# Kernel tuning notes

Measured on AMD Instinct MI355X. Metric: run time of the kernel, lower is better.

## Reference

```python
import jax, jax.numpy as jnp
import numpy as np

N_NODES = 20000
N_EDGES = 320000
IN_DIM = 256
OUT_DIM = 256
N_HEADS = 4
D_K = OUT_DIM // N_HEADS
N_NTYPES = 4
N_RELS = 8
SQRT_DK = float(np.sqrt(D_K))


def setup_inputs() -> dict:
    key = jax.random.key(0)
    ks = jax.random.split(key, 12)
    xav = lambda k, shape, fan: jax.random.normal(k, shape, jnp.float32) * (1.0 / np.sqrt(fan))
    return {
        "h": jax.random.normal(ks[0], (N_NODES, IN_DIM), jnp.float32),
        "k_linears": xav(ks[1], (N_NTYPES, IN_DIM, OUT_DIM), IN_DIM),
        "q_linears": xav(ks[2], (N_NTYPES, IN_DIM, OUT_DIM), IN_DIM),
        "v_linears": xav(ks[3], (N_NTYPES, IN_DIM, OUT_DIM), IN_DIM),
        "a_linears": xav(ks[4], (N_NTYPES, OUT_DIM, OUT_DIM), OUT_DIM),
        "relation_att": xav(ks[5], (N_RELS, N_HEADS, D_K, D_K), D_K),
        "relation_msg": xav(ks[6], (N_RELS, N_HEADS, D_K, D_K), D_K),
        "relation_pri": jnp.ones((N_RELS, N_HEADS), jnp.float32),
        "skip": jnp.ones((N_NTYPES,), jnp.float32),
        "node_type": jax.random.randint(ks[7], (N_NODES,), 0, N_NTYPES),
        "etype": jnp.sort(jax.random.randint(ks[8], (N_EDGES,), 0, N_RELS)),
        "row_idx": jax.random.randint(ks[9], (N_EDGES,), 0, N_NODES),
        "col_idx": jax.random.randint(ks[10], (N_EDGES,), 0, N_NODES),
    }


def _typed_matmul(x, W, node_type):
    # x: [N, in], W: [T, in, out] -> per-node-type projection [N, out]
    all_t = jnp.einsum("ni,tio->tno", x, W)  # [T, N, out]
    return all_t[node_type, jnp.arange(x.shape[0])]


def reference(h, k_linears, q_linears, v_linears, a_linears,
              relation_att, relation_msg, relation_pri, skip,
              node_type, etype, row_idx, col_idx):
    n = h.shape[0]
    # per-node-type K/Q/V projections -> [N, H, d_k]
    k = _typed_matmul(h, k_linears, node_type).reshape(n, N_HEADS, D_K)
    q = _typed_matmul(h, q_linears, node_type).reshape(n, N_HEADS, D_K)
    v = _typed_matmul(h, v_linears, node_type).reshape(n, N_HEADS, D_K)

    # per-relation transforms computed at node granularity, gathered per edge
    q_att = jnp.einsum("nhd,rhde->rnhe", q, relation_att)  # [R, N, H, d_k]
    v_msg = jnp.einsum("nhd,rhde->rnhe", v, relation_msg)  # [R, N, H, d_k]

    aw_q_edge = q_att[etype, col_idx]   # [E, H, d_k]  (dst-side q transformed by rel att)
    msg_edge = v_msg[etype, row_idx]    # [E, H, d_k]  (src-side v transformed by rel msg)

    # attention score: <rel_att @ q_dst, k_src> * pri_r / sqrt(d_k)  -> [E, H]
    attn_score = jnp.sum(aw_q_edge * k[row_idx], axis=-1)
    score = attn_score * (relation_pri[etype] / SQRT_DK)

    # edge softmax over incoming edges of each destination node
    m = jax.ops.segment_max(score, col_idx, num_segments=n)       # [N, H]
    ex = jnp.exp(score - m[col_idx])                              # [E, H]
    denom = jax.ops.segment_sum(ex, col_idx, num_segments=n)      # [N, H]
    alpha = ex / denom[col_idx]                                   # [E, H]

    agg = jax.ops.segment_sum(alpha[..., None] * msg_edge, col_idx,
                              num_segments=n)                     # [N, H, d_k]
    agg = agg.reshape(n, OUT_DIM)

    # output per-node-type projection scaled by sigmoid(skip[type])
    out = _typed_matmul(agg, a_linears, node_type)
    out = jax.nn.sigmoid(skip)[node_type][:, None] * out
    return out
```

## Files before the change

kernel.cpp:

```cpp
#include <hip/hip_runtime.h>

static constexpr int NN  = 20000;
static constexpr int NE  = 320000;
static constexpr int NTY = 4;
static constexpr int NRL = 8;
static constexpr int NB  = NRL * NN;

static constexpr int ZB   = (NB + NN * 4 + 255) / 256;
static constexpr int CB   = (NN + 255) / 256;
static constexpr int WSEG = 192;
static constexpr int ASEG = 64;
static constexpr int RSEG = 32;

typedef short bf16x8 __attribute__((ext_vector_type(8)));
typedef float f32x4  __attribute__((ext_vector_type(4)));
typedef unsigned short u16x4 __attribute__((ext_vector_type(4)));

__device__ __forceinline__ unsigned short f2bf(float f) {
  unsigned u = __float_as_uint(f);
  u += 0x7fffu + ((u >> 16) & 1u);
  return (unsigned short)(u >> 16);
}
__device__ __forceinline__ float bf2f(unsigned short b) {
  return __uint_as_float(((unsigned)b) << 16);
}
__device__ __forceinline__ f32x4 mfma16(bf16x8 a, bf16x8 b, f32x4 c) {
  return __builtin_amdgcn_mfma_f32_16x16x32_bf16(a, b, c, 0, 0, 0);
}

__global__ void k_prep_all(const float* __restrict__ Wk, const float* __restrict__ Wq,
                           const float* __restrict__ Wv, const float* __restrict__ Wa,
                           const float* __restrict__ ratt, const float* __restrict__ rmsg,
                           const int* __restrict__ ntype,
                           int* bcnt, float* denom, int* c4p,
                           unsigned short* Wt, unsigned short* At,
                           unsigned short* Att, unsigned short* Mt) {
  __shared__ float tl[64][65];
  __shared__ int cc[4];
  int b = blockIdx.x, tid = threadIdx.x;
  if (b < ZB) {
    int i = b * 256 + tid;
    if (i < NB) bcnt[i] = 0;
    else if (i < NB + NN * 4) denom[i - NB] = 0.f;
    return;
  }
  b -= ZB;
  if (b < CB) {
    if (tid < 4) cc[tid] = 0;
    __syncthreads();
    int i = b * 256 + tid;
    if (i < NN) atomicAdd(&cc[ntype[i]], 1);
    __syncthreads();
    if (tid < 4) c4p[b * 4 + tid] = cc[tid];
    return;
  }
  b -= CB;
  int r4 = tid >> 6, c = tid & 63;
  if (b < WSEG) {
    int mat = b >> 4, tile = b & 15;
    int t = mat / 3, w = mat % 3;
    const float* src = (w == 0) ? Wk : (w == 1) ? Wq : Wv;
    src += (size_t)t * 65536;
    int ti = (tile >> 2) * 64, tj = (tile & 3) * 64;
#pragma unroll
    for (int p = 0; p < 16; ++p) {
      int row = p * 4 + r4;
      tl[row][c] = src[(size_t)(ti + row) * 256 + tj + c];
    }
    __syncthreads();
#pragma unroll
    for (int p = 0; p < 16; ++p) {
      int jr = p * 4 + r4;
      Wt[((size_t)(t * 768 + w * 256 + tj + jr)) * 256 + ti + c] = f2bf(tl[c][jr]);
    }
    return;
  }
  b -= WSEG;
  if (b < ASEG) {
    int t = b >> 4, tile = b & 15;
    int ti = (tile >> 2) * 64, tj = (tile & 3) * 64;
#pragma unroll
    for (int p = 0; p < 16; ++p) {
      int row = p * 4 + r4;
      tl[row][c] = Wa[(size_t)(t * 256 + ti + row) * 256 + tj + c];
    }
    __syncthreads();
#pragma unroll
    for (int p = 0; p < 16; ++p) {
      int jr = p * 4 + r4;
      At[((size_t)(t * 256 + tj + jr)) * 256 + ti + c] = f2bf(tl[c][jr]);
    }
    return;
  }
  b -= ASEG;
  {
    int rh = b;
#pragma unroll
    for (int p = 0; p < 16; ++p) {
      int d = p * 4 + r4;
      tl[d][c] = ratt[(size_t)rh * 4096 + d * 64 + c];
    }
    __syncthreads();
#pragma unroll
    for (int p = 0; p < 16; ++p) {
      int e = p * 4 + r4;
      Att[(size_t)rh * 4096 + e * 64 + c] = f2bf(tl[c][e]);
    }
    __syncthreads();
#pragma unroll
    for (int p = 0; p < 16; ++p) {
      int d = p * 4 + r4;
      tl[d][c] = rmsg[(size_t)rh * 4096 + d * 64 + c];
    }
    __syncthreads();
#pragma unroll
    for (int p = 0; p < 16; ++p) {
      int e = p * 4 + r4;
      Mt[(size_t)rh * 4096 + e * 64 + c] = f2bf(tl[c][e]);
    }
  }
}

__global__ void k_meta(const int* __restrict__ c4p, int* toff, int* ncur,
                       int* mt64_t, int* mt64_m, int* gcnt) {
  __shared__ int c4[4];
  __shared__ int ts[5];
  if (threadIdx.x < 4) {
    int s = 0;
    for (int b = 0; b < CB; ++b) s += c4p[b * 4 + threadIdx.x];
    c4[threadIdx.x] = s;
  }
  __syncthreads();
  if (threadIdx.x == 0) {
    int s = 0, s2 = 0;
    for (int t = 0; t < NTY; ++t) {
      toff[t] = s; ncur[t] = s; s += c4[t];
      ts[t] = s2; s2 += (c4[t] + 63) >> 6;
    }
    toff[NTY] = s; ts[NTY] = s2; gcnt[0] = s2;
  }
  __syncthreads();
  int n64 = ts[4];
  for (int i = threadIdx.x; i < n64; i += 256) {
    int t = 0;
    while (t < 3 && i >= ts[t + 1]) ++t;
    mt64_t[i] = t; mt64_m[i] = i - ts[t];
  }
}
__global__ void k_nscatter(const int* __restrict__ key, int* cur,
                           int* nperm, int* inv) {
  int i = blockIdx.x * 256 + threadIdx.x;
  if (i < NN) {
    int p = atomicAdd(&cur[key[i]], 1);
    nperm[p] = i;
    inv[i] = p;
  }
}

__global__ void k_bcount(const int* __restrict__ etyp, const int* __restrict__ coli,
                         const int* __restrict__ inv, int* bcnt) {
  int e = blockIdx.x * 256 + threadIdx.x;
  if (e < NE) atomicAdd(&bcnt[etyp[e] * NN + inv[coli[e]]], 1);
}
__global__ void k_scan1(const int* cnt, int* off, int* psum) {
  __shared__ int sm[256];
  int i = blockIdx.x * 256 + threadIdx.x;
  int v = cnt[i];
  sm[threadIdx.x] = v;
  __syncthreads();
  for (int d = 1; d < 256; d <<= 1) {
    int t = (threadIdx.x >= d) ? sm[threadIdx.x - d] : 0;
    __syncthreads();
    sm[threadIdx.x] += t;
    __syncthreads();
  }
  off[i] = sm[threadIdx.x] - v;
  if (threadIdx.x == 255) psum[blockIdx.x] = sm[255];
}
__global__ void k_scan2(int* psum) {
  __shared__ int sm[1024];
  int t = threadIdx.x;
  int v = (t < 625) ? psum[t] : 0;
  sm[t] = v;
  __syncthreads();
  for (int d = 1; d < 1024; d <<= 1) {
    int x = (t >= d) ? sm[t - d] : 0;
    __syncthreads();
    sm[t] += x;
    __syncthreads();
  }
  if (t < 625) psum[t] = sm[t] - v;
}
__global__ void k_scan3(int* off, int* cur, const int* psum) {
  int i = blockIdx.x * 256 + threadIdx.x;
  int v = off[i] + psum[blockIdx.x];
  off[i] = v; cur[i] = v;
  if (i == 0) off[NB] = NE;
}
__global__ void k_escatter(const int* __restrict__ etyp, const int* __restrict__ rowi,
                           const int* __restrict__ coli, const int* __restrict__ inv,
                           int* cur, int* je) {
  int e = blockIdx.x * 256 + threadIdx.x;
  if (e >= NE) return;
  int bin = etyp[e] * NN + inv[coli[e]];
  int j = atomicAdd(&cur[bin], 1);
  je[j] = inv[rowi[e]];
}

__global__ __launch_bounds__(256) void k_gemm_kqv(
    const float* __restrict__ hsrc, const unsigned short* __restrict__ Wt,
    const int* __restrict__ nperm, const int* __restrict__ toff,
    const int* __restrict__ mt64_t, const int* __restrict__ mt64_m,
    const int* __restrict__ gcnt,
    unsigned short* __restrict__ kvb, unsigned short* __restrict__ qb) {
  __shared__ unsigned short bs[16][264];
  int mtile = blockIdx.x / 3, chunk = blockIdx.x % 3;
  if (mtile >= gcnt[0]) return;
  int wave = threadIdx.x >> 6, lane = threadIdx.x & 63;
  int t = mt64_t[mtile], tm = mt64_m[mtile];
  int base = toff[t], cnt = toff[t + 1] - base;
  int lr = lane & 15, kq = lane >> 4;
  int arow = tm * 64 + wave * 16 + lr;
  int prow = base + (arow < cnt ? arow : cnt - 1);
  int node = nperm[prow];
  const float* ap = hsrc + (size_t)node * 256 + kq * 8;
  bf16x8 af[8];
#pragma unroll
  for (int s = 0; s < 8; ++s) {
    f32x4 x0 = *(const f32x4*)(ap + s * 32);
    f32x4 x1 = *(const f32x4*)(ap + s * 32 + 4);
    bf16x8 o;
    o[0] = (short)f2bf(x0[0]); o[1] = (short)f2bf(x0[1]);
    o[2] = (short)f2bf(x0[2]); o[3] = (short)f2bf(x0[3]);
    o[4] = (short)f2bf(x1[0]); o[5] = (short)f2bf(x1[1]);
    o[6] = (short)f2bf(x1[2]); o[7] = (short)f2bf(x1[3]);
    af[s] = o;
  }
  int pr[4]; bool wr[4];
#pragma unroll
  for (int i = 0; i < 4; ++i) {
    int crow = tm * 64 + wave * 16 + kq * 4 + i;
    wr[i] = crow < cnt;
    pr[i] = base + (wr[i] ? crow : 0);
  }
  int sc = threadIdx.x >> 4;
  int seg = threadIdx.x & 15;
  for (int tt = 0; tt < 16; ++tt) {
    int tn = chunk * 16 + tt;
    const unsigned short* wsrc = Wt + ((size_t)(t * 768 + tn * 16 + sc)) * 256 + seg * 16;
    __syncthreads();
    *(bf16x8*)&bs[sc][seg * 16]     = *(const bf16x8*)wsrc;
    *(bf16x8*)&bs[sc][seg * 16 + 8] = *(const bf16x8*)(wsrc + 8);
    __syncthreads();
    f32x4 acc = {0.f, 0.f, 0.f, 0.f};
#pragma unroll
    for (int s = 0; s < 8; ++s)
      acc = mfma16(af[s], *(const bf16x8*)&bs[lr][kq * 8 + s * 32], acc);
    int ccol = tn * 16 + lr;
#pragma unroll
    for (int i = 0; i < 4; ++i) {
      if (wr[i]) {
        unsigned short v = f2bf(acc[i]);
        if (ccol < 256)
          kvb[(size_t)pr[i] * 512 + (ccol >> 6) * 128 + (ccol & 63)] = v;
        else if (ccol < 512)
          qb[(size_t)pr[i] * 256 + (ccol - 256)] = v;
        else {
          int c = ccol - 512;
          kvb[(size_t)pr[i] * 512 + (c >> 6) * 128 + 64 + (c & 63)] = v;
        }
      }
    }
  }
}

__global__ __launch_bounds__(256) void k_mega(
    const int* __restrict__ boff, const int* __restrict__ je,
    const unsigned short* __restrict__ qb, const unsigned short* __restrict__ kvb,
    const unsigned short* __restrict__ Att, const unsigned short* __restrict__ Mt,
    const float* __restrict__ pri, unsigned short* __restrict__ aggh,
    float* __restrict__ denom) {
  __shared__ float qsh[4][32][68];
  int dt = blockIdx.x >> 2, quarter = blockIdx.x & 3;
  int h = threadIdx.x >> 6, lane = threadIdx.x & 63;
  int lr16 = lane & 15, kq4 = lane >> 4;
  int lr32 = lane & 31, kq1 = lane >> 5;
  int r0 = quarter * 2;
  float dtot = 0.f;
  f32x4 C[2][4] = {{{0.f,0.f,0.f,0.f},{0.f,0.f,0.f,0.f},{0.f,0.f,0.f,0.f},{0.f,0.f,0.f,0.f}},
                   {{0.f,0.f,0.f,0.f},{0.f,0.f,0.f,0.f},{0.f,0.f,0.f,0.f},{0.f,0.f,0.f,0.f}}};
  for (int rr = 0; rr < 2; ++rr) {
    int r = r0 + rr;
    int rh = r * 4 + h;
    int bin = r * NN + dt * 32 + lr32;
    int b0 = boff[bin], b1 = boff[bin + 1];
#pragma unroll
    for (int hf = 0; hf < 2; ++hf) {
      const unsigned short* ap = qb + (size_t)(dt * 32 + hf * 16 + lr16) * 256 + h * 64 + kq4 * 8;
      bf16x8 aq0 = *(const bf16x8*)ap;
      bf16x8 aq1 = *(const bf16x8*)(ap + 32);
#pragma unroll
      for (int tn = 0; tn < 4; ++tn) {
        const unsigned short* bp = Att + ((rh * 64 + tn * 16 + lr16) * 64) + kq4 * 8;
        f32x4 a = {0.f, 0.f, 0.f, 0.f};
        a = mfma16(aq0, *(const bf16x8*)bp, a);
        a = mfma16(aq1, *(const bf16x8*)(bp + 32), a);
#pragma unroll
        for (int i = 0; i < 4; ++i)
          qsh[h][hf * 16 + kq4 * 4 + i][tn * 16 + lr16] = a[i];
      }
    }
    float qt[32];
#pragma unroll
    for (int m = 0; m < 32; m += 4) {
      f32x4 v = *(const f32x4*)&qsh[h][lr32][kq1 * 32 + m];
      qt[m] = v[0]; qt[m + 1] = v[1]; qt[m + 2] = v[2]; qt[m + 3] = v[3];
    }
    float acc[32];
#pragma unroll
    for (int m = 0; m < 32; ++m) acc[m] = 0.f;
    float prs = pri[rh] * 0.125f;
    int src_next = (b0 < b1) ? je[b0] : 0;
    for (int j = b0; j < b1; ++j) {
      int src = src_next;
      if (j + 1 < b1) src_next = je[j + 1];
      const unsigned short* kp = kvb + (size_t)src * 512 + h * 128 + kq1 * 32;
      bf16x8 k0 = *(const bf16x8*)kp;
      bf16x8 k1 = *(const bf16x8*)(kp + 8);
      bf16x8 k2 = *(const bf16x8*)(kp + 16);
      bf16x8 k3 = *(const bf16x8*)(kp + 24);
      bf16x8 v0 = *(const bf16x8*)(kp + 64);
      bf16x8 v1 = *(const bf16x8*)(kp + 72);
      bf16x8 v2 = *(const bf16x8*)(kp + 80);
      bf16x8 v3 = *(const bf16x8*)(kp + 88);
      float s = 0.f;
#pragma unroll
      for (int m = 0; m < 8; ++m) {
        s += qt[m]      * bf2f((unsigned short)k0[m]);
        s += qt[8 + m]  * bf2f((unsigned short)k1[m]);
        s += qt[16 + m] * bf2f((unsigned short)k2[m]);
        s += qt[24 + m] * bf2f((unsigned short)k3[m]);
      }
      s += __shfl_xor(s, 32);
      float ex = __expf(s * prs);
      dtot += ex;
#pragma unroll
      for (int m = 0; m < 8; ++m) {
        acc[m]      += ex * bf2f((unsigned short)v0[m]);
        acc[8 + m]  += ex * bf2f((unsigned short)v1[m]);
        acc[16 + m] += ex * bf2f((unsigned short)v2[m]);
        acc[24 + m] += ex * bf2f((unsigned short)v3[m]);
      }
    }
#pragma unroll
    for (int m = 0; m < 32; m += 4) {
      f32x4 v = {acc[m], acc[m + 1], acc[m + 2], acc[m + 3]};
      *(f32x4*)&qsh[h][lr32][kq1 * 32 + m] = v;
    }
#pragma unroll
    for (int hf = 0; hf < 2; ++hf) {
      bf16x8 m0, m1;
#pragma unroll
      for (int m = 0; m < 8; ++m) {
        m0[m] = (short)f2bf(qsh[h][hf * 16 + lr16][kq4 * 8 + m]);
        m1[m] = (short)f2bf(qsh[h][hf * 16 + lr16][32 + kq4 * 8 + m]);
      }
#pragma unroll
      for (int tn = 0; tn < 4; ++tn) {
        const unsigned short* bp = Mt + ((rh * 64 + tn * 16 + lr16) * 64) + kq4 * 8;
        C[hf][tn] = mfma16(m0, *(const bf16x8*)bp, C[hf][tn]);
        C[hf][tn] = mfma16(m1, *(const bf16x8*)(bp + 32), C[hf][tn]);
      }
    }
  }
  if (kq1 == 0) atomicAdd(&denom[(dt * 32 + lr32) * 4 + h], dtot);
#pragma unroll
  for (int hf = 0; hf < 2; ++hf)
#pragma unroll
    for (int tn = 0; tn < 4; ++tn)
#pragma unroll
      for (int i = 0; i < 4; ++i)
        aggh[((size_t)quarter * NN + dt * 32 + hf * 16 + kq4 * 4 + i) * 256 +
             h * 64 + tn * 16 + lr16] = f2bf(C[hf][tn][i]);
}

__global__ __launch_bounds__(256) void k_gemm_out(
    const unsigned short* __restrict__ aggh, const float* __restrict__ denom,
    const unsigned short* __restrict__ At,
    const int* __restrict__ nperm, const int* __restrict__ toff,
    const int* __restrict__ mt64_t, const int* __restrict__ mt64_m,
    const int* __restrict__ gcnt,
    const float* __restrict__ skip, float* __restrict__ out) {
  __shared__ unsigned short bs[16][264];
  int mtile = blockIdx.x >> 1, chunk = blockIdx.x & 1;
  if (mtile >= gcnt[0]) return;
  int wave = threadIdx.x >> 6, lane = threadIdx.x & 63;
  int t = mt64_t[mtile], tm = mt64_m[mtile];
  int base = toff[t], cnt = toff[t + 1] - base;
  int lr = lane & 15, kq = lane >> 4;
  int arow = tm * 64 + wave * 16 + lr;
  int prow = base + (arow < cnt ? arow : cnt - 1);
  float dn[4];
#pragma unroll
  for (int hh = 0; hh < 4; ++hh) {
    float d = denom[prow * 4 + hh];
    dn[hh] = d > 0.f ? 1.f / d : 0.f;
  }
  const unsigned short* g = aggh + (size_t)prow * 256 + kq * 8;
  bf16x8 af[8];
#pragma unroll
  for (int s = 0; s < 8; ++s) {
    bf16x8 x0 = *(const bf16x8*)(g + s * 32);
    bf16x8 x1 = *(const bf16x8*)(g + (size_t)NN * 256 + s * 32);
    bf16x8 x2 = *(const bf16x8*)(g + (size_t)2 * NN * 256 + s * 32);
    bf16x8 x3 = *(const bf16x8*)(g + (size_t)3 * NN * 256 + s * 32);
    float dv = dn[(kq * 8 + s * 32) >> 6];
#pragma unroll
    for (int m = 0; m < 8; ++m)
      af[s][m] = (short)f2bf((bf2f((unsigned short)x0[m]) + bf2f((unsigned short)x1[m]) +
                              bf2f((unsigned short)x2[m]) + bf2f((unsigned short)x3[m])) * dv);
  }
  int nd[4]; bool wr[4];
#pragma unroll
  for (int i = 0; i < 4; ++i) {
    int crow = tm * 64 + wave * 16 + kq * 4 + i;
    wr[i] = crow < cnt;
    nd[i] = nperm[base + (wr[i] ? crow : 0)];
  }
  float sg = 1.f / (1.f + __expf(-skip[t]));
  int sc = threadIdx.x >> 4;
  int seg = threadIdx.x & 15;
  for (int tt = 0; tt < 8; ++tt) {
    int tn = chunk * 8 + tt;
    const unsigned short* wsrc = At + ((size_t)(t * 256 + tn * 16 + sc)) * 256 + seg * 16;
    __syncthreads();
    *(bf16x8*)&bs[sc][seg * 16]     = *(const bf16x8*)wsrc;
    *(bf16x8*)&bs[sc][seg * 16 + 8] = *(const bf16x8*)(wsrc + 8);
    __syncthreads();
    f32x4 acc = {0.f, 0.f, 0.f, 0.f};
#pragma unroll
    for (int s = 0; s < 8; ++s)
      acc = mfma16(af[s], *(const bf16x8*)&bs[lr][kq * 8 + s * 32], acc);
    int ccol = tn * 16 + lr;
#pragma unroll
    for (int i = 0; i < 4; ++i)
      if (wr[i]) out[nd[i] * 256 + ccol] = acc[i] * sg;
  }
}

extern "C" void kernel_launch(void* const* d_in, const int* in_sizes, int n_in,
                              void* d_out, int out_size, void* d_ws, size_t ws_size,
                              hipStream_t stream) {
  (void)in_sizes; (void)n_in; (void)out_size; (void)ws_size;
  const float* h    = (const float*)d_in[0];
  const float* Wk   = (const float*)d_in[1];
  const float* Wq   = (const float*)d_in[2];
  const float* Wv   = (const float*)d_in[3];
  const float* Wa   = (const float*)d_in[4];
  const float* ratt = (const float*)d_in[5];
  const float* rmsg = (const float*)d_in[6];
  const float* pri  = (const float*)d_in[7];
  const float* skp  = (const float*)d_in[8];
  const int* ntype  = (const int*)d_in[9];
  const int* etyp   = (const int*)d_in[10];
  const int* rowi   = (const int*)d_in[11];
  const int* coli   = (const int*)d_in[12];
  float* out = (float*)d_out;

  char* p = (char*)d_ws;
  auto alloc = [&](size_t bytes) {
    void* q = (void*)p;
    p += (bytes + 255) & ~(size_t)255;
    return q;
  };
  unsigned short* Wt   = (unsigned short*)alloc((size_t)4 * 768 * 256 * 2);
  unsigned short* At   = (unsigned short*)alloc((size_t)4 * 256 * 256 * 2);
  unsigned short* Att  = (unsigned short*)alloc((size_t)32 * 4096 * 2);
  unsigned short* Mt   = (unsigned short*)alloc((size_t)32 * 4096 * 2);
  unsigned short* kvb  = (unsigned short*)alloc((size_t)NN * 512 * 2);
  unsigned short* qb   = (unsigned short*)alloc((size_t)NN * 256 * 2);
  unsigned short* aggh = (unsigned short*)alloc((size_t)4 * NN * 256 * 2);
  float* denom = (float*)alloc((size_t)NN * 4 * 4);
  int* toff   = (int*)alloc(32);
  int* ncur   = (int*)alloc(16);
  int* c4p    = (int*)alloc((size_t)CB * 4 * 4);
  int* nperm  = (int*)alloc((size_t)NN * 4);
  int* inv    = (int*)alloc((size_t)NN * 4);
  int* bcnt   = (int*)alloc((size_t)NB * 4);
  int* boff   = (int*)alloc((size_t)(NB + 1) * 4);
  int* bcur   = (int*)alloc((size_t)NB * 4);
  int* psum   = (int*)alloc((size_t)625 * 4);
  int* je     = (int*)alloc((size_t)NE * 4);
  int* mt64_t = (int*)alloc((size_t)324 * 4);
  int* mt64_m = (int*)alloc((size_t)324 * 4);
  int* gcnt   = (int*)alloc(32);

  k_prep_all<<<ZB + CB + WSEG + ASEG + RSEG, 256, 0, stream>>>(
      Wk, Wq, Wv, Wa, ratt, rmsg, ntype, bcnt, denom, c4p, Wt, At, Att, Mt);
  k_meta<<<1, 256, 0, stream>>>(c4p, toff, ncur, mt64_t, mt64_m, gcnt);
  k_nscatter<<<CB, 256, 0, stream>>>(ntype, ncur, nperm, inv);

  k_bcount<<<(NE + 255) / 256, 256, 0, stream>>>(etyp, coli, inv, bcnt);
  k_scan1<<<625, 256, 0, stream>>>(bcnt, boff, psum);
  k_scan2<<<1, 1024, 0, stream>>>(psum);
  k_scan3<<<625, 256, 0, stream>>>(boff, bcur, psum);
  k_escatter<<<(NE + 255) / 256, 256, 0, stream>>>(etyp, rowi, coli, inv, bcur, je);

  k_gemm_kqv<<<960, 256, 0, stream>>>(h, Wt, nperm, toff, mt64_t, mt64_m, gcnt, kvb, qb);
  k_mega<<<2500, 256, 0, stream>>>(boff, je, qb, kvb, Att, Mt, pri, aggh, denom);
  k_gemm_out<<<640, 256, 0, stream>>>(aggh, denom, At, nperm, toff, mt64_t, mt64_m, gcnt,
                                      skp, out);
}
```

Baseline: 330.9 us.

## Load GEMM weight fragments directly from global and use memset for zeroing

Both projection GEMM kernels stop staging each 16-column weight slice through shared memory and drop the two barriers per slice. Each lane now reads its bf16x8 weight fragments straight from global memory and relies on L1/L2 to serve the reuse across waves. The zero-initialisation of the bin counts and softmax denominators moves out of the fused prep kernel into two hipMemsetAsync calls. This removes LDS traffic and barriers, at the cost of redundant global and cache reads by all four waves, plus two extra launches.

```diff
diff --git a/kernel.cpp b/kernel.cpp
--- a/kernel.cpp
+++ b/kernel.cpp
@@ -6,7 +6,6 @@
 static constexpr int NRL = 8;
 static constexpr int NB  = NRL * NN;
 
-static constexpr int ZB   = (NB + NN * 4 + 255) / 256;
 static constexpr int CB   = (NN + 255) / 256;
 static constexpr int WSEG = 192;
 static constexpr int ASEG = 64;
@@ -32,19 +31,12 @@
                            const float* __restrict__ Wv, const float* __restrict__ Wa,
                            const float* __restrict__ ratt, const float* __restrict__ rmsg,
                            const int* __restrict__ ntype,
-                           int* bcnt, float* denom, int* c4p,
+                           int* c4p,
                            unsigned short* Wt, unsigned short* At,
                            unsigned short* Att, unsigned short* Mt) {
   __shared__ float tl[64][65];
   __shared__ int cc[4];
   int b = blockIdx.x, tid = threadIdx.x;
-  if (b < ZB) {
-    int i = b * 256 + tid;
-    if (i < NB) bcnt[i] = 0;
-    else if (i < NB + NN * 4) denom[i - NB] = 0.f;
-    return;
-  }
-  b -= ZB;
   if (b < CB) {
     if (tid < 4) cc[tid] = 0;
     __syncthreads();
@@ -213,7 +205,6 @@
     const int* __restrict__ mt64_t, const int* __restrict__ mt64_m,
     const int* __restrict__ gcnt,
     unsigned short* __restrict__ kvb, unsigned short* __restrict__ qb) {
-  __shared__ unsigned short bs[16][264];
   int mtile = blockIdx.x / 3, chunk = blockIdx.x % 3;
   if (mtile >= gcnt[0]) return;
   int wave = threadIdx.x >> 6, lane = threadIdx.x & 63;
@@ -243,19 +234,13 @@
     wr[i] = crow < cnt;
     pr[i] = base + (wr[i] ? crow : 0);
   }
-  int sc = threadIdx.x >> 4;
-  int seg = threadIdx.x & 15;
   for (int tt = 0; tt < 16; ++tt) {
     int tn = chunk * 16 + tt;
-    const unsigned short* wsrc = Wt + ((size_t)(t * 768 + tn * 16 + sc)) * 256 + seg * 16;
-    __syncthreads();
-    *(bf16x8*)&bs[sc][seg * 16]     = *(const bf16x8*)wsrc;
-    *(bf16x8*)&bs[sc][seg * 16 + 8] = *(const bf16x8*)(wsrc + 8);
-    __syncthreads();
+    const unsigned short* bptr = Wt + ((size_t)(t * 768 + tn * 16 + lr)) * 256 + kq * 8;
     f32x4 acc = {0.f, 0.f, 0.f, 0.f};
 #pragma unroll
     for (int s = 0; s < 8; ++s)
-      acc = mfma16(af[s], *(const bf16x8*)&bs[lr][kq * 8 + s * 32], acc);
+      acc = mfma16(af[s], *(const bf16x8*)(bptr + s * 32), acc);
     int ccol = tn * 16 + lr;
 #pragma unroll
     for (int i = 0; i < 4; ++i) {
@@ -391,7 +376,6 @@
     const int* __restrict__ mt64_t, const int* __restrict__ mt64_m,
     const int* __restrict__ gcnt,
     const float* __restrict__ skip, float* __restrict__ out) {
-  __shared__ unsigned short bs[16][264];
   int mtile = blockIdx.x >> 1, chunk = blockIdx.x & 1;
   if (mtile >= gcnt[0]) return;
   int wave = threadIdx.x >> 6, lane = threadIdx.x & 63;
@@ -428,19 +412,13 @@
     nd[i] = nperm[base + (wr[i] ? crow : 0)];
   }
   float sg = 1.f / (1.f + __expf(-skip[t]));
-  int sc = threadIdx.x >> 4;
-  int seg = threadIdx.x & 15;
   for (int tt = 0; tt < 8; ++tt) {
     int tn = chunk * 8 + tt;
-    const unsigned short* wsrc = At + ((size_t)(t * 256 + tn * 16 + sc)) * 256 + seg * 16;
-    __syncthreads();
-    *(bf16x8*)&bs[sc][seg * 16]     = *(const bf16x8*)wsrc;
-    *(bf16x8*)&bs[sc][seg * 16 + 8] = *(const bf16x8*)(wsrc + 8);
-    __syncthreads();
+    const unsigned short* bptr = At + ((size_t)(t * 256 + tn * 16 + lr)) * 256 + kq * 8;
     f32x4 acc = {0.f, 0.f, 0.f, 0.f};
 #pragma unroll
     for (int s = 0; s < 8; ++s)
-      acc = mfma16(af[s], *(const bf16x8*)&bs[lr][kq * 8 + s * 32], acc);
+      acc = mfma16(af[s], *(const bf16x8*)(bptr + s * 32), acc);
     int ccol = tn * 16 + lr;
 #pragma unroll
     for (int i = 0; i < 4; ++i)
@@ -495,8 +473,11 @@
   int* mt64_m = (int*)alloc((size_t)324 * 4);
   int* gcnt   = (int*)alloc(32);
 
-  k_prep_all<<<ZB + CB + WSEG + ASEG + RSEG, 256, 0, stream>>>(
-      Wk, Wq, Wv, Wa, ratt, rmsg, ntype, bcnt, denom, c4p, Wt, At, Att, Mt);
+  hipMemsetAsync(bcnt, 0, (size_t)NB * 4, stream);
+  hipMemsetAsync(denom, 0, (size_t)NN * 4 * 4, stream);
+
+  k_prep_all<<<CB + WSEG + ASEG + RSEG, 256, 0, stream>>>(
+      Wk, Wq, Wv, Wa, ratt, rmsg, ntype, c4p, Wt, At, Att, Mt);
   k_meta<<<1, 256, 0, stream>>>(c4p, toff, ncur, mt64_t, mt64_m, gcnt);
   k_nscatter<<<CB, 256, 0, stream>>>(ntype, ncur, nperm, inv);
 
```

Result: slower. 392.3 us (+18.6%).
